# Performance work log

Measured on AMD Instinct MI355X. Metric: run time of the kernel, lower is better.

The kernel has to match this reference:

```python
import jax, jax.numpy as jnp
import numpy as np

QMIN, QMAX = -128, 127  # signed int8 range


def setup_inputs() -> dict:
    key = jax.random.key(0)
    k_x, k_w, k_b = jax.random.split(key, 3)
    N, C_in, H, W = 32, 128, 56, 56
    C_out, kH, kW = 256, 3, 3
    # int8-valued tensors carried as int32 (jax-friendly); values in [-128, 127]
    x = jax.random.randint(k_x, (N, C_in, H, W), 0, 256, dtype=jnp.int32) - 128
    weight = jax.random.randint(k_w, (C_out, C_in, kH, kW), 0, 256, dtype=jnp.int32) - 128
    # int32 bias, already quantized with scale s_in * s_w
    bias = jax.random.randint(k_b, (C_out,), -(2 ** 14), 2 ** 14, dtype=jnp.int32)
    return {
        "x": x,
        "weight": weight,
        "bias": bias,
        "input_scale": jnp.float32(0.02),
        "weight_scale": jnp.float32(0.005),
        "output_scale": jnp.float32(0.05),
        "input_zero_point": jnp.int32(-5),
        "output_zero_point": jnp.int32(3),
    }


def reference(x, weight, bias, input_scale, weight_scale, output_scale,
              input_zero_point, output_zero_point):
    # Dequant-style integer conv: shift input by its zero point (weights are
    # symmetric, zero point 0), accumulate in fp32 (stands in for int32 acc).
    x_f = (x - input_zero_point).astype(jnp.float32)
    w_f = weight.astype(jnp.float32)
    acc = jax.lax.conv_general_dilated(
        x_f, w_f,
        window_strides=(1, 1),
        padding=((1, 1), (1, 1)),
        dimension_numbers=("NCHW", "OIHW", "NCHW"),
    )
    acc = acc + bias.astype(jnp.float32)[None, :, None, None]
    # Requantize: scale fusion + output zero point, round, clamp to int8.
    requant_scale = input_scale * weight_scale / output_scale
    y = acc * requant_scale + output_zero_point.astype(jnp.float32)
    y_q = jnp.clip(jnp.round(y), QMIN, QMAX).astype(jnp.int8)
    return y_q
```

## Files before the change

### kernel.cpp

```cpp
#include <hip/hip_runtime.h>
#include <stdint.h>


#define NB 32
#define CI 128
#define HH 56
#define WW 56
#define CO 256
#define SPA (HH * WW)
#define HP 58
#define WP 64
#define XP2_BYTES (NB * HP * WP * CI)
#define BP_BYTES (9 * 2 * 4 * CO * 16)
#define ABUF (4 * 8192)

typedef int v4i __attribute__((ext_vector_type(4)));

__global__ __launch_bounds__(256) void prep_kernel(
    const int* __restrict__ x, const int* __restrict__ wgt,
    const int* __restrict__ bias, const int* __restrict__ zpi,
    int8_t* __restrict__ xp2, int8_t* __restrict__ bp, int* __restrict__ BG)
{
    __shared__ int sm[1824];
    const int tid = threadIdx.x, bid = blockIdx.x;
    const int zp = *zpi;
    const int zp4 = (zp & 255) * 0x01010101;

    if (bid < HH * NB) {
        const int n = bid / HH, h = bid % HH;
        #pragma unroll
        for (int it = 0; it < 7; ++it) {
            int j = tid + it * 256;
            int ci = j / 14, w4 = j - ci * 14;
            const v4i v = *(const v4i*)(x + ((n * CI + ci) * HH + h) * WW + w4 * 4);
            sm[w4 * 130 + ci] = (v.x & 255) | ((v.y & 255) << 8) |
                                ((v.z & 255) << 16) | (v.w << 24);
        }
        __syncthreads();
        int* od = (int*)xp2 + (n * HP + h + 1) * (WP * CI / 4);
        #pragma unroll
        for (int it = 0; it < 8; ++it) {
            int j = tid + it * 256;
            int widx = j >> 5, ci4 = j & 31;
            int val = zp4;
            if (widx >= 1 && widx <= WW) {
                int w = widx - 1;
                int base = (w >> 2) * 130 + ci4 * 4;
                int sh = (w & 3) * 8;
                val = ((sm[base] >> sh) & 0xff) | (((sm[base+1] >> sh) & 0xff) << 8) |
                      (((sm[base+2] >> sh) & 0xff) << 16) | ((sm[base+3] >> sh) << 24);
            }
            od[j ^ ((widx & 7) << 2)] = val;
        }
    } else if (bid < HH * NB + 2 * NB) {
        const int z = bid - HH * NB;
        const int n = z >> 1, hidx = (z & 1) ? (HP - 1) : 0;
        int* od = (int*)xp2 + (n * HP + hidx) * (WP * CI / 4);
        #pragma unroll
        for (int it = 0; it < 8; ++it) od[tid + it * 256] = zp4;
    } else {
        const int co = bid - (HH * NB + 2 * NB);
        for (int j = tid; j < 1152; j += 256) sm[j] = wgt[co * 1152 + j];
        __syncthreads();
        for (int j = tid; j < 288; j += 256) {
            int j4 = j & 3, q = (j >> 2) & 3, c64 = (j >> 4) & 1, t = j >> 5;
            int ci = c64 * 64 + q * 16 + j4 * 4;
            int b0 = sm[(ci + 0) * 9 + t] & 255, b1 = sm[(ci + 1) * 9 + t] & 255;
            int b2 = sm[(ci + 2) * 9 + t] & 255, b3 = sm[(ci + 3) * 9 + t];
            ((int*)bp)[((t * 2 + c64) * 4 + q) * 1024 + co * 4 + j4] =
                b0 | (b1 << 8) | (b2 << 16) | (b3 << 24);
        }
        if (tid < 9) {
            int s = 0;
            for (int ci = 0; ci < CI; ++ci) s += sm[ci * 9 + tid];
            sm[1152 + tid] = s;
        }
        __syncthreads();
        if (tid == 0) {
            int s9 = 0;
            for (int t = 0; t < 9; ++t) s9 += sm[1152 + t];
            BG[co] = bias[co] - zp * s9;
        }
    }
}

__global__ __launch_bounds__(256) void qconv_mfma(
    const int8_t* __restrict__ xp2, const int8_t* __restrict__ bp,
    const int* __restrict__ BG,
    const float* __restrict__ si, const float* __restrict__ sw,
    const float* __restrict__ so, const int* __restrict__ zpo,
    int* __restrict__ out)
{
    const int tid  = threadIdx.x, lane = tid & 63, wid = tid >> 6;
    const int quad = lane >> 4, lo16 = lane & 15;
    const int bid  = blockIdx.x;
    const int xcd  = bid & 7, idx = bid >> 3;
    const int n    = xcd * 4 + (idx & 3);
    const int s2   = idx >> 2;
    const int cw   = wid * 64;

    __shared__ __attribute__((aligned(16))) int8_t Asm[ABUF];

    const int8_t* src0 = xp2 + (((size_t)n * HP + 2 * s2) << 13);
    #pragma unroll
    for (int k = 0; k < 8; ++k) {
        const int u = wid + 4 * k;
        __builtin_amdgcn_global_load_lds(
            (const __attribute__((address_space(1))) void*)(src0 + (u << 10) + lane * 16),
            (__attribute__((address_space(3))) void*)(&Asm[u << 10]), 16, 0, 0);
    }

    int bgv[4];
    #pragma unroll
    for (int ct = 0; ct < 4; ++ct) bgv[ct] = BG[cw + ct * 16 + lo16];
    const float rs = (*si) * (*sw) / (*so);
    const float zo = (float)(*zpo);

    int boff[7], sw3[7];
    #pragma unroll
    for (int mt = 0; mt < 7; ++mt) {
        const int ml = mt * 16 + lo16;
        const int srow = ml / 56, scol = ml - srow * 56;
        boff[mt] = srow * 8192 + scol * 128 + quad * 16;
        int t0 = ((scol + 0) & 7) << 4, t1 = ((scol + 1) & 7) << 4,
            t2 = ((scol + 2) & 7) << 4;
        sw3[mt] = t0 | (t1 << 8) | (t2 << 16);
    }

    const int8_t* bwav = bp + ((size_t)quad << 12) + ((cw + lo16) << 4);

    int* optr = out + ((size_t)n * CO + cw + lo16) * SPA + quad * 4;

    #define BLOAD(tp) {                                                        \
        const int8_t* bb = bwav + ((tp) * 8 << 12);                            \
        asm volatile("" : "+v"(bb));                                           \
        bt[tp][0] = *(const v4i*)(bb);                                         \
        bt[tp][1] = *(const v4i*)(bb + 256);                                   \
        bt[tp][2] = *(const v4i*)(bb + 512);                                   \
        bt[tp][3] = *(const v4i*)(bb + 768);                                   \
        bt[tp][4] = *(const v4i*)(bb + 16384);                                 \
        bt[tp][5] = *(const v4i*)(bb + 16384 + 256);                           \
        bt[tp][6] = *(const v4i*)(bb + 16384 + 512);                           \
        bt[tp][7] = *(const v4i*)(bb + 16384 + 768);                           \
    }

    #define AADDR(tp, mt) \
        ((boff[mt] + ((tp) / 3) * 8192 + ((tp) % 3) * 128) ^ \
         ((sw3[mt] >> (8 * ((tp) % 3))) & 0x70))

    v4i bt[9][8];
    BLOAD(0);

    v4i acc[7][4];
    #pragma unroll
    for (int mt = 0; mt < 7; ++mt)
        #pragma unroll
        for (int ct = 0; ct < 4; ++ct) acc[mt][ct] = (v4i){0, 0, 0, 0};

    __syncthreads();

    v4i a0p[2], a1p[2];
    { const int p = AADDR(0, 0);
      a0p[0] = *(const v4i*)(Asm + p); a1p[0] = *(const v4i*)(Asm + (p ^ 64)); }

    #pragma unroll
    for (int it = 0; it < 63; ++it) {
        const int tp = it / 7, mt = it % 7;
        if (mt == 0 && tp + 1 <= 8) BLOAD(tp + 1);
        if (it + 1 < 63) {
            const int tp1 = (it + 1) / 7, mt1 = (it + 1) % 7;
            const int p = AADDR(tp1, mt1);
            a0p[(it + 1) & 1] = *(const v4i*)(Asm + p);
            a1p[(it + 1) & 1] = *(const v4i*)(Asm + (p ^ 64));
        }
        const v4i a0 = a0p[it & 1], a1 = a1p[it & 1];
        #pragma unroll
        for (int ct = 0; ct < 4; ++ct)
            acc[mt][ct] = __builtin_amdgcn_mfma_i32_16x16x64_i8(a0, bt[tp][ct], acc[mt][ct], 0, 0, 0);
        #pragma unroll
        for (int ct = 0; ct < 4; ++ct)
            acc[mt][ct] = __builtin_amdgcn_mfma_i32_16x16x64_i8(a1, bt[tp][4 + ct], acc[mt][ct], 0, 0, 0);
    }
    #undef BLOAD
    #undef AADDR

    const int m0 = s2 * 112;
    #pragma unroll
    for (int mt = 0; mt < 7; ++mt) {
        #pragma unroll
        for (int ct = 0; ct < 4; ++ct) {
            v4i vv;
            #pragma unroll
            for (int i4 = 0; i4 < 4; ++i4) {
                float yv = rintf((float)(acc[mt][ct][i4] + bgv[ct]) * rs + zo);
                yv = fminf(fmaxf(yv, -128.f), 127.f);
                vv[i4] = (int)yv;
            }
            *(v4i*)(optr + ct * 16 * SPA + m0 + mt * 16) = vv;
        }
    }
}

extern "C" void kernel_launch(void* const* d_in, const int* in_sizes, int n_in,
                              void* d_out, int out_size, void* d_ws, size_t ws_size,
                              hipStream_t stream) {
    const int*   x    = (const int*)d_in[0];
    const int*   wgt  = (const int*)d_in[1];
    const int*   bias = (const int*)d_in[2];
    const float* si   = (const float*)d_in[3];
    const float* sw   = (const float*)d_in[4];
    const float* so   = (const float*)d_in[5];
    const int*   zpi  = (const int*)d_in[6];
    const int*   zpo  = (const int*)d_in[7];
    int* out = (int*)d_out;

    int8_t* xp2 = (int8_t*)d_ws;
    int8_t* bp  = xp2 + XP2_BYTES;
    int*    bg  = (int*)(bp + BP_BYTES);

    prep_kernel<<<HH * NB + 2 * NB + CO, 256, 0, stream>>>(x, wgt, bias, zpi, xp2, bp, bg);
    qconv_mfma<<<896, 256, 0, stream>>>(xp2, bp, bg, si, sw, so, zpo, out);
}
```

Before: 203.1 us.

## Split conv blocks into 2-wave halves over output channels, double-buffer B fragments

Each block now has 2 waves covering 128 output channels instead of 4 waves covering 256, so the grid doubles and each block loads its input tile into LDS with 16 loads per wave. The fully register-resident B fragment array (9 taps) is replaced by a 2-slot double buffer, and the swizzle is computed from the address instead of precomputed tables, cutting VGPR use to target 2 waves per EU. The cost is that each input tile is now staged into LDS twice, once per channel-half block.

Measured after the change: 191.3 us. 1.06x faster.

```diff
diff --git a/kernel.cpp b/kernel.cpp
--- a/kernel.cpp
+++ b/kernel.cpp
@@ -84,7 +84,9 @@
     }
 }
 
-__global__ __launch_bounds__(256) void qconv_mfma(
+__global__ __launch_bounds__(128)
+__attribute__((amdgpu_waves_per_eu(2)))
+void qconv_mfma(
     const int8_t* __restrict__ xp2, const int8_t* __restrict__ bp,
     const int* __restrict__ BG,
     const float* __restrict__ si, const float* __restrict__ sw,
@@ -96,15 +98,16 @@
     const int bid  = blockIdx.x;
     const int xcd  = bid & 7, idx = bid >> 3;
     const int n    = xcd * 4 + (idx & 3);
-    const int s2   = idx >> 2;
-    const int cw   = wid * 64;
+    const int cb   = (idx >> 2) & 1;
+    const int s2   = idx >> 3;
+    const int cw   = cb * 128 + wid * 64;
 
     __shared__ __attribute__((aligned(16))) int8_t Asm[ABUF];
 
     const int8_t* src0 = xp2 + (((size_t)n * HP + 2 * s2) << 13);
     #pragma unroll
-    for (int k = 0; k < 8; ++k) {
-        const int u = wid + 4 * k;
+    for (int k = 0; k < 16; ++k) {
+        const int u = wid + 2 * k;
         __builtin_amdgcn_global_load_lds(
             (const __attribute__((address_space(1))) void*)(src0 + (u << 10) + lane * 16),
             (__attribute__((address_space(3))) void*)(&Asm[u << 10]), 16, 0, 0);
@@ -116,15 +119,12 @@
     const float rs = (*si) * (*sw) / (*so);
     const float zo = (float)(*zpo);
 
-    int boff[7], sw3[7];
+    int boff[7];
     #pragma unroll
     for (int mt = 0; mt < 7; ++mt) {
         const int ml = mt * 16 + lo16;
         const int srow = ml / 56, scol = ml - srow * 56;
         boff[mt] = srow * 8192 + scol * 128 + quad * 16;
-        int t0 = ((scol + 0) & 7) << 4, t1 = ((scol + 1) & 7) << 4,
-            t2 = ((scol + 2) & 7) << 4;
-        sw3[mt] = t0 | (t1 << 8) | (t2 << 16);
     }
 
     const int8_t* bwav = bp + ((size_t)quad << 12) + ((cw + lo16) << 4);
@@ -134,21 +134,21 @@
     #define BLOAD(tp) {                                                        \
         const int8_t* bb = bwav + ((tp) * 8 << 12);                            \
         asm volatile("" : "+v"(bb));                                           \
-        bt[tp][0] = *(const v4i*)(bb);                                         \
-        bt[tp][1] = *(const v4i*)(bb + 256);                                   \
-        bt[tp][2] = *(const v4i*)(bb + 512);                                   \
-        bt[tp][3] = *(const v4i*)(bb + 768);                                   \
-        bt[tp][4] = *(const v4i*)(bb + 16384);                                 \
-        bt[tp][5] = *(const v4i*)(bb + 16384 + 256);                           \
-        bt[tp][6] = *(const v4i*)(bb + 16384 + 512);                           \
-        bt[tp][7] = *(const v4i*)(bb + 16384 + 768);                           \
-    }
-
-    #define AADDR(tp, mt) \
-        ((boff[mt] + ((tp) / 3) * 8192 + ((tp) % 3) * 128) ^ \
-         ((sw3[mt] >> (8 * ((tp) % 3))) & 0x70))
-
-    v4i bt[9][8];
+        bt[(tp) & 1][0] = *(const v4i*)(bb);                                   \
+        bt[(tp) & 1][1] = *(const v4i*)(bb + 256);                             \
+        bt[(tp) & 1][2] = *(const v4i*)(bb + 512);                             \
+        bt[(tp) & 1][3] = *(const v4i*)(bb + 768);                             \
+        bt[(tp) & 1][4] = *(const v4i*)(bb + 16384);                           \
+        bt[(tp) & 1][5] = *(const v4i*)(bb + 16384 + 256);                     \
+        bt[(tp) & 1][6] = *(const v4i*)(bb + 16384 + 512);                     \
+        bt[(tp) & 1][7] = *(const v4i*)(bb + 16384 + 768);                     \
+    }
+
+    #define AADDR(tp, mt) ({                                                   \
+        const int off_ = boff[mt] + ((tp) / 3) * 8192 + ((tp) % 3) * 128;      \
+        off_ ^ (((off_ >> 7) & 7) << 4); })
+
+    v4i bt[2][8];
     BLOAD(0);
 
     v4i acc[7][4];
@@ -168,18 +168,17 @@
         const int tp = it / 7, mt = it % 7;
         if (mt == 0 && tp + 1 <= 8) BLOAD(tp + 1);
         if (it + 1 < 63) {
-            const int tp1 = (it + 1) / 7, mt1 = (it + 1) % 7;
-            const int p = AADDR(tp1, mt1);
+            const int p = AADDR((it + 1) / 7, (it + 1) % 7);
             a0p[(it + 1) & 1] = *(const v4i*)(Asm + p);
             a1p[(it + 1) & 1] = *(const v4i*)(Asm + (p ^ 64));
         }
         const v4i a0 = a0p[it & 1], a1 = a1p[it & 1];
         #pragma unroll
         for (int ct = 0; ct < 4; ++ct)
-            acc[mt][ct] = __builtin_amdgcn_mfma_i32_16x16x64_i8(a0, bt[tp][ct], acc[mt][ct], 0, 0, 0);
+            acc[mt][ct] = __builtin_amdgcn_mfma_i32_16x16x64_i8(a0, bt[tp & 1][ct], acc[mt][ct], 0, 0, 0);
         #pragma unroll
         for (int ct = 0; ct < 4; ++ct)
-            acc[mt][ct] = __builtin_amdgcn_mfma_i32_16x16x64_i8(a1, bt[tp][4 + ct], acc[mt][ct], 0, 0, 0);
+            acc[mt][ct] = __builtin_amdgcn_mfma_i32_16x16x64_i8(a1, bt[tp & 1][4 + ct], acc[mt][ct], 0, 0, 0);
     }
     #undef BLOAD
     #undef AADDR
@@ -219,5 +218,5 @@
     int*    bg  = (int*)(bp + BP_BYTES);
 
     prep_kernel<<<HH * NB + 2 * NB + CO, 256, 0, stream>>>(x, wgt, bias, zpi, xp2, bp, bg);
-    qconv_mfma<<<896, 256, 0, stream>>>(xp2, bp, bg, si, sw, so, zpo, out);
+    qconv_mfma<<<1792, 128, 0, stream>>>(xp2, bp, bg, si, sw, so, zpo, out);
 }
```
